# Optimization experiments

Hardware: AMD Instinct MI355X
Metric: run time of the kernel (lower is better)

## Reference

```python
import jax, jax.numpy as jnp
import numpy as np

N_EMBD = 1024
N_HEADS = 16
HEAD_DIM = N_EMBD // N_HEADS


def setup_inputs() -> dict:
    key = jax.random.key(0)
    ks = jax.random.split(key, 6)
    s = 1.0 / np.sqrt(N_EMBD)
    x = jax.random.normal(ks[0], (2, 2048, N_EMBD), dtype=jnp.float32)
    # torch Linear weights are [out, in]; y = x @ W.T
    Wk = jax.random.uniform(ks[1], (N_EMBD, N_EMBD), jnp.float32, -s, s)
    Wq = jax.random.uniform(ks[2], (N_EMBD, N_EMBD), jnp.float32, -s, s)
    Wv = jax.random.uniform(ks[3], (N_EMBD, N_EMBD), jnp.float32, -s, s)
    Wp = jax.random.uniform(ks[4], (N_EMBD, N_EMBD), jnp.float32, -s, s)
    bp = jax.random.uniform(ks[5], (N_EMBD,), jnp.float32, -s, s)
    return {"x": x, "Wq": Wq, "Wk": Wk, "Wv": Wv, "Wp": Wp, "bp": bp}


def reference(x, Wq, Wk, Wv, Wp, bp):
    B, T, C = x.shape
    H, D = N_HEADS, HEAD_DIM
    # projections (torch Linear: x @ W.T), reshape to [B, H, T, D]
    q = (x @ Wq.T).reshape(B, T, H, D).transpose(0, 2, 1, 3)
    k = (x @ Wk.T).reshape(B, T, H, D).transpose(0, 2, 1, 3)
    v = (x @ Wv.T).reshape(B, T, H, D).transpose(0, 2, 1, 3)
    # scaled causal attention, full [B,H,T,T] scores (faithful to original)
    att = jnp.einsum('bhqd,bhkd->bhqk', q, k) * (D ** -0.5)
    causal = jnp.tril(jnp.ones((T, T), dtype=bool))
    att = jnp.where(causal[None, None], att, -jnp.inf)
    att = jax.nn.softmax(att, axis=-1)
    out = jnp.einsum('bhqk,bhkd->bhqd', att, v)
    out = out.transpose(0, 2, 1, 3).reshape(B, T, C)
    return out @ Wp.T + bp
```

## Files before the change

kernel.cpp:

```cpp
#include <hip/hip_runtime.h>

typedef __bf16 bf16;
typedef __bf16 bf16x8 __attribute__((ext_vector_type(8)));
typedef float f32x4 __attribute__((ext_vector_type(4)));

typedef __attribute__((address_space(1))) const void as1_void;
typedef __attribute__((address_space(3))) void as3_void;

#define DEV __device__ __forceinline__
#define NEG_BIG (-1.0e30f)


DEV void async_load16(const void* g, void* l) {
  __builtin_amdgcn_global_load_lds((as1_void*)g, (as3_void*)l, 16, 0, 0);
}
DEV bf16x8 load8(const bf16* p) { bf16x8 v; __builtin_memcpy(&v, p, 16); return v; }
DEV void store8(bf16* p, bf16x8 v) { __builtin_memcpy(p, &v, 16); }
DEV float fexp2(float x) { float r; asm("v_exp_f32 %0, %1" : "=v"(r) : "v"(x)); return r; }

DEV int sniff_bf16(const unsigned short* __restrict__ xr) {
  const int lane = threadIdx.x & 63;
  const unsigned short w = xr[lane * 2];
  const int e = (w >> 7) & 0xFF;
  const bool sane = ((w & 0x7FFF) == 0) || (e >= 97 && e <= 157);
  return __popcll(__ballot(sane)) >= 48;
}

struct ConvArgs {
  const void* src[6];
  bf16* dst[6];
  int n[6];
};

__global__ __launch_bounds__(256) void convert_kernel(ConvArgs a) {
  const int isbf = sniff_bf16((const unsigned short*)a.src[0]);
  const int t = blockIdx.y;
  const int n = a.n[t];
  bf16* d = a.dst[t];
  const int stride = gridDim.x * 256 * 8;
  if (isbf) {
    const bf16* s = (const bf16*)a.src[t];
    for (int i = (blockIdx.x * 256 + threadIdx.x) * 8; i < n; i += stride)
      store8(d + i, load8(s + i));
  } else {
    const float* s = (const float*)a.src[t];
    for (int i = (blockIdx.x * 256 + threadIdx.x) * 8; i < n; i += stride) {
      float tmp[8];
      __builtin_memcpy(tmp, s + i, 32);
      bf16x8 v;
#pragma unroll
      for (int j = 0; j < 8; ++j) v[j] = (bf16)tmp[j];
      store8(d + i, v);
    }
  }
}

DEV void gemm_core_128_p(const bf16* A, const bf16* W, const int K, int m0, int n0,
                         f32x4 (&acc)[4][4]) {
  __shared__ alignas(16) bf16 As[3][128 * 32];
  __shared__ alignas(16) bf16 Bs[3][128 * 32];
  const int tid = threadIdx.x;
  const int lane = tid & 63;
  const int wid = tid >> 6;
  const int wm = (wid >> 1) << 6;
  const int wn = (wid & 1) << 6;
  const int lr = lane & 15;
  const int lg = lane >> 4;

  size_t srcA[2], srcB[2];
  int ldsoff[2];
#pragma unroll
  for (int it = 0; it < 2; ++it) {
    const int lin = it * 256 + tid;
    const int lr2 = lin >> 3, c = lin & 7;
    const int u = c ^ (lr2 & 7);
    const int r = lr2 * 2 + (u >> 2);
    const int g = u & 3;
    srcA[it] = (size_t)(m0 + r) * K + (size_t)(g * 8);
    srcB[it] = (size_t)(n0 + r) * K + (size_t)(g * 8);
    ldsoff[it] = lin * 8;
  }
  int offA[4], offB[4];
#pragma unroll
  for (int i = 0; i < 4; ++i) {
    const int r = wm + i * 16 + lr;
    const int cc = (lg | ((r & 1) << 2)) ^ ((r >> 1) & 7);
    offA[i] = (((r >> 1) << 3) | cc) * 8;
  }
#pragma unroll
  for (int j = 0; j < 4; ++j) {
    const int r = wn + j * 16 + lr;
    const int cc = (lg | ((r & 1) << 2)) ^ ((r >> 1) & 7);
    offB[j] = (((r >> 1) << 3) | cc) * 8;
  }

  const f32x4 zero = {0.f, 0.f, 0.f, 0.f};
#pragma unroll
  for (int i = 0; i < 4; ++i)
#pragma unroll
    for (int j = 0; j < 4; ++j) acc[i][j] = zero;

  const int nt = K >> 5;

  auto stage = [&](int buf, int t) {
    const size_t k0 = (size_t)(t << 5);
#pragma unroll
    for (int it = 0; it < 2; ++it) {
      async_load16(A + srcA[it] + k0, &As[buf][0] + ldsoff[it]);
      async_load16(W + srcB[it] + k0, &Bs[buf][0] + ldsoff[it]);
    }
  };

  auto compute = [&](int buf) {
    const bf16* as = &As[buf][0];
    const bf16* bs = &Bs[buf][0];
    bf16x8 af[4], bfr[4];
#pragma unroll
    for (int i = 0; i < 4; ++i) af[i] = load8(as + offA[i]);
#pragma unroll
    for (int j = 0; j < 4; ++j) bfr[j] = load8(bs + offB[j]);
    __builtin_amdgcn_s_setprio(1);
#pragma unroll
    for (int i = 0; i < 4; ++i)
#pragma unroll
      for (int j = 0; j < 4; ++j)
        acc[i][j] = __builtin_amdgcn_mfma_f32_16x16x32_bf16(af[i], bfr[j], acc[i][j], 0, 0, 0);
    __builtin_amdgcn_s_setprio(0);
  };

  stage(0, 0);
  stage(1, 1);
  int b0 = 0, b1 = 1, b2 = 2;
  for (int t = 0; t < nt; ++t) {
    if (t + 1 < nt) asm volatile("s_waitcnt vmcnt(4)" ::: "memory");
    else            asm volatile("s_waitcnt vmcnt(0)" ::: "memory");
    __builtin_amdgcn_s_barrier();
    if (t + 2 < nt) stage(b2, t + 2);
    compute(b0);
    const int tmp = b0; b0 = b1; b1 = b2; b2 = tmp;
  }
}

DEV void gemm_core_128x64_p(const bf16* A, const bf16* W, const int K, int m0, int n0,
                            f32x4 (&acc)[4][2]) {
  __shared__ alignas(16) bf16 As[3][128 * 32];
  __shared__ alignas(16) bf16 Bs[3][64 * 32];
  const int tid = threadIdx.x;
  const int lane = tid & 63;
  const int wid = tid >> 6;
  const int wm = (wid >> 1) << 6;
  const int wn = (wid & 1) << 5;
  const int lr = lane & 15;
  const int lg = lane >> 4;

  size_t srcA[2], srcB;
  int ldsoffA[2], ldsoffB;
#pragma unroll
  for (int it = 0; it < 2; ++it) {
    const int lin = it * 256 + tid;
    const int lr2 = lin >> 3, c = lin & 7;
    const int u = c ^ (lr2 & 7);
    srcA[it] = (size_t)(m0 + lr2 * 2 + (u >> 2)) * K + (size_t)((u & 3) * 8);
    ldsoffA[it] = lin * 8;
  }
  {
    const int lin = tid;
    const int lr2 = lin >> 3, c = lin & 7;
    const int u = c ^ (lr2 & 7);
    srcB = (size_t)(n0 + lr2 * 2 + (u >> 2)) * K + (size_t)((u & 3) * 8);
    ldsoffB = lin * 8;
  }
  int offA[4], offB[2];
#pragma unroll
  for (int i = 0; i < 4; ++i) {
    const int r = wm + i * 16 + lr;
    const int cc = (lg | ((r & 1) << 2)) ^ ((r >> 1) & 7);
    offA[i] = (((r >> 1) << 3) | cc) * 8;
  }
#pragma unroll
  for (int j = 0; j < 2; ++j) {
    const int r = wn + j * 16 + lr;
    const int cc = (lg | ((r & 1) << 2)) ^ ((r >> 1) & 7);
    offB[j] = (((r >> 1) << 3) | cc) * 8;
  }

  const f32x4 zero = {0.f, 0.f, 0.f, 0.f};
#pragma unroll
  for (int i = 0; i < 4; ++i)
#pragma unroll
    for (int j = 0; j < 2; ++j) acc[i][j] = zero;

  const int nt = K >> 5;

  auto stage = [&](int buf, int t) {
    const size_t k0 = (size_t)(t << 5);
#pragma unroll
    for (int it = 0; it < 2; ++it)
      async_load16(A + srcA[it] + k0, &As[buf][0] + ldsoffA[it]);
    async_load16(W + srcB + k0, &Bs[buf][0] + ldsoffB);
  };

  auto compute = [&](int buf) {
    const bf16* as = &As[buf][0];
    const bf16* bs = &Bs[buf][0];
    bf16x8 af[4], bfr[2];
#pragma unroll
    for (int i = 0; i < 4; ++i) af[i] = load8(as + offA[i]);
#pragma unroll
    for (int j = 0; j < 2; ++j) bfr[j] = load8(bs + offB[j]);
    __builtin_amdgcn_s_setprio(1);
#pragma unroll
    for (int i = 0; i < 4; ++i)
#pragma unroll
      for (int j = 0; j < 2; ++j)
        acc[i][j] = __builtin_amdgcn_mfma_f32_16x16x32_bf16(af[i], bfr[j], acc[i][j], 0, 0, 0);
    __builtin_amdgcn_s_setprio(0);
  };

  stage(0, 0);
  stage(1, 1);
  int b0 = 0, b1 = 1, b2 = 2;
  for (int t = 0; t < nt; ++t) {
    if (t + 1 < nt) asm volatile("s_waitcnt vmcnt(3)" ::: "memory");
    else            asm volatile("s_waitcnt vmcnt(0)" ::: "memory");
    __builtin_amdgcn_s_barrier();
    if (t + 2 < nt) stage(b2, t + 2);
    compute(b0);
    const int tmp = b0; b0 = b1; b1 = b2; b2 = tmp;
  }
}

DEV size_t frag_idx(int row, int col) {
  return ((size_t)(((col >> 5) * 4 + ((row >> 4) & 3)) * 64 + ((col >> 3) & 3) * 16 + (row & 15)) << 3)
         | (size_t)(col & 7);
}

__global__ __launch_bounds__(256) void qkv_proj_kernel(
    const bf16* __restrict__ x, const bf16* __restrict__ Wq,
    const bf16* __restrict__ Wk, const bf16* __restrict__ Wv,
    bf16* __restrict__ q_ws, bf16* __restrict__ k_ws, bf16* __restrict__ vt_ws) {
  const int L = blockIdx.x;
  const int xcd = L & 7;
  const int i2 = L >> 3;
  const int m0 = (xcd * 4 + (i2 & 3)) << 7;
  const int rest = i2 >> 2;
  const int n0 = (rest & 7) << 7;
  const int mode = rest >> 3;
  const bf16* W = (mode == 0) ? Wq : (mode == 1) ? Wk : Wv;
  f32x4 acc[4][4];
  gemm_core_128_p(x, W, 1024, m0, n0, acc);

  const int tid = threadIdx.x;
  const int lane = tid & 63, wid = tid >> 6;
  const int wm = (wid >> 1) << 6, wn = (wid & 1) << 6;
  const int lr = lane & 15, lg = lane >> 4;
  bf16* out = (mode == 0) ? q_ws : (mode == 1) ? k_ws : vt_ws;
  const float scale = (mode == 0) ? 0.18033688011112042f : 1.0f;
#pragma unroll
  for (int i = 0; i < 4; ++i) {
#pragma unroll
    for (int r = 0; r < 4; ++r) {
      const int m = m0 + wm + i * 16 + lg * 4 + r;
      const int b = m >> 11, t = m & 2047;
#pragma unroll
      for (int j = 0; j < 4; ++j) {
        const int n = n0 + wn + j * 16 + lr;
        const int h = n >> 6, d = n & 63;
        const float v = acc[i][j][r] * scale;
        const size_t base = ((size_t)(b * 16 + h) << 17) + ((size_t)(t >> 6) << 12);
        const size_t idx = base + ((mode < 2) ? frag_idx(t & 63, d) : frag_idx(d, t & 63));
        out[idx] = (bf16)v;
      }
    }
  }
}

__global__ __launch_bounds__(256, 4) void attn_kernel(
    const bf16* __restrict__ q_ws, const bf16* __restrict__ k_ws,
    const bf16* __restrict__ vt_ws, bf16* __restrict__ a_ws) {
  const int L = blockIdx.x;
  const int bh = (L & 7) * 4 + ((L >> 3) & 3);
  const int qt = 31 - (L >> 5);
  const int tid = threadIdx.x;
  const int lane = tid & 63, w = tid >> 6;
  const int lr = lane & 15, lg = lane >> 4;
  const int fo = lg * 16 + lr;

  __shared__ alignas(16) bf16 Ks[2][4096];
  __shared__ alignas(16) bf16 Ps[4][16 * 72];
  bf16* ps = &Ps[w][0];

  const size_t hb = (size_t)bh << 17;
  const int b = bh >> 4, h = bh & 15;
  const f32x4 zero = {0.f, 0.f, 0.f, 0.f};
  const bf16* kbase = k_ws + hb;
  const bf16* vbase = vt_ws + hb;
  const size_t qtb = hb + ((size_t)qt << 12);

  bf16x8 aq[2];
#pragma unroll
  for (int c2 = 0; c2 < 2; ++c2)
    aq[c2] = load8(q_ws + qtb + (size_t)(((c2 * 4 + w) * 64 + fo) << 3));

  f32x4 o_acc[4];
#pragma unroll
  for (int j = 0; j < 4; ++j) o_acc[j] = zero;
  float lsum[4] = {0.f, 0.f, 0.f, 0.f};

  const int nt = qt + 1;
  auto ktof = [&](int s) { return (s == 0) ? qt : (s - 1); };

  auto stage = [&](int buf, int s) {
    const int kt = ktof(s);
    const bf16* kg = kbase + ((size_t)kt << 12);
#pragma unroll
    for (int it = 0; it < 2; ++it) {
      const int lin = it * 256 + tid;
      async_load16(kg + lin * 8, &Ks[buf][0] + lin * 8);
    }
  };

  auto step = [&](int buf, int kt, bool diag) {
    const bf16* ks = &Ks[buf][0];
    const bf16* vg = vbase + ((size_t)kt << 12);
    bf16x8 bv[2][4];
#pragma unroll
    for (int c2 = 0; c2 < 2; ++c2)
#pragma unroll
      for (int j = 0; j < 4; ++j)
        bv[c2][j] = load8(vg + (size_t)(((c2 * 4 + j) * 64 + fo) << 3));

    f32x4 s[4];
    __builtin_amdgcn_s_setprio(1);
#pragma unroll
    for (int j = 0; j < 4; ++j) {
      s[j] = __builtin_amdgcn_mfma_f32_16x16x32_bf16(
          aq[0], load8(ks + (size_t)(((0 * 4 + j) * 64 + fo) << 3)), zero, 0, 0, 0);
      s[j] = __builtin_amdgcn_mfma_f32_16x16x32_bf16(
          aq[1], load8(ks + (size_t)(((1 * 4 + j) * 64 + fo) << 3)), s[j], 0, 0, 0);
    }
    __builtin_amdgcn_s_setprio(0);
    float p[4][4];
#pragma unroll
    for (int j = 0; j < 4; ++j) {
#pragma unroll
      for (int r = 0; r < 4; ++r) {
        float v = s[j][r];
        if (diag && (j * 16 + lr) > (w * 16 + lg * 4 + r)) v = NEG_BIG;
        p[j][r] = fexp2(v);
      }
    }
#pragma unroll
    for (int r = 0; r < 4; ++r)
      lsum[r] += (p[0][r] + p[1][r]) + (p[2][r] + p[3][r]);
#pragma unroll
    for (int j = 0; j < 4; ++j)
#pragma unroll
      for (int r = 0; r < 4; ++r)
        ps[(lg * 4 + r) * 72 + j * 16 + lr] = (bf16)p[j][r];
    __builtin_amdgcn_s_setprio(1);
#pragma unroll
    for (int c2 = 0; c2 < 2; ++c2) {
      const bf16x8 ap = load8(ps + lr * 72 + c2 * 32 + lg * 8);
#pragma unroll
      for (int j = 0; j < 4; ++j)
        o_acc[j] = __builtin_amdgcn_mfma_f32_16x16x32_bf16(ap, bv[c2][j], o_acc[j], 0, 0, 0);
    }
    __builtin_amdgcn_s_setprio(0);
  };

  stage(0, 0);
  int cur = 0;
  for (int t = 0; t < nt; ++t) {
    asm volatile("s_waitcnt vmcnt(0)" ::: "memory");
    __builtin_amdgcn_s_barrier();
    if (t + 1 < nt) stage(cur ^ 1, t + 1);
    step(cur, ktof(t), t == 0);
    cur ^= 1;
  }

#pragma unroll
  for (int r = 0; r < 4; ++r) {
    float v = lsum[r];
#pragma unroll
    for (int off = 1; off < 16; off <<= 1) v += __shfl_xor(v, off, 64);
    const float inv = 1.f / v;
    const int t = qt * 64 + w * 16 + lg * 4 + r;
#pragma unroll
    for (int j = 0; j < 4; ++j) {
      const size_t idx = (((size_t)(b * 2048 + t)) << 10) | (size_t)(h * 64 + j * 16 + lr);
      a_ws[idx] = (bf16)(o_acc[j][r] * inv);
    }
  }
}

__global__ __launch_bounds__(256) void out_proj_kernel(
    const bf16* __restrict__ A, const bf16* __restrict__ Wp,
    const bf16* __restrict__ bp, void* __restrict__ out,
    const unsigned short* __restrict__ xraw) {
  const int L = blockIdx.x;
  const int xcd = L & 7;
  const int i2 = L >> 3;
  const int m0 = (xcd * 4 + (i2 & 3)) << 7;
  const int n0 = (i2 >> 2) << 6;
  f32x4 acc[4][2];
  gemm_core_128x64_p(A, Wp, 1024, m0, n0, acc);

  const int tid = threadIdx.x;
  const int lane = tid & 63, wid = tid >> 6;
  const int wm = (wid >> 1) << 6, wn = (wid & 1) << 5;
  const int lr = lane & 15, lg = lane >> 4;
  const int isbf = sniff_bf16(xraw);
#pragma unroll
  for (int i = 0; i < 4; ++i) {
#pragma unroll
    for (int r = 0; r < 4; ++r) {
      const int m = m0 + wm + i * 16 + lg * 4 + r;
#pragma unroll
      for (int j = 0; j < 2; ++j) {
        const int n = n0 + wn + j * 16 + lr;
        const float v = acc[i][j][r] + (float)bp[n];
        const size_t idx = ((size_t)m << 10) | (size_t)n;
        if (isbf) ((bf16*)out)[idx] = (bf16)v;
        else      ((float*)out)[idx] = v;
      }
    }
  }
}

extern "C" void kernel_launch(void* const* d_in, const int* in_sizes, int n_in,
                              void* d_out, int out_size, void* d_ws, size_t ws_size,
                              hipStream_t stream) {
  (void)in_sizes; (void)n_in; (void)out_size;
  if (ws_size < (50u << 20)) return;

  char* ws = (char*)d_ws;
  bf16* q_ws  = (bf16*)(ws);
  bf16* k_ws  = (bf16*)(ws + (8u << 20));
  bf16* vt_ws = (bf16*)(ws + (16u << 20));
  bf16* a_ws  = (bf16*)(ws + (24u << 20));
  bf16* xc    = (bf16*)(ws + (32u << 20));
  bf16* Wqc   = (bf16*)(ws + (40u << 20));
  bf16* Wkc   = (bf16*)(ws + (42u << 20));
  bf16* Wvc   = (bf16*)(ws + (44u << 20));
  bf16* Wpc   = (bf16*)(ws + (46u << 20));
  bf16* bpc   = (bf16*)(ws + (48u << 20));

  ConvArgs ca;
  ca.src[0] = d_in[0]; ca.dst[0] = xc;  ca.n[0] = 4096 * 1024;
  ca.src[1] = d_in[1]; ca.dst[1] = Wqc; ca.n[1] = 1024 * 1024;
  ca.src[2] = d_in[2]; ca.dst[2] = Wkc; ca.n[2] = 1024 * 1024;
  ca.src[3] = d_in[3]; ca.dst[3] = Wvc; ca.n[3] = 1024 * 1024;
  ca.src[4] = d_in[4]; ca.dst[4] = Wpc; ca.n[4] = 1024 * 1024;
  ca.src[5] = d_in[5]; ca.dst[5] = bpc; ca.n[5] = 1024;
  convert_kernel<<<dim3(512, 6), 256, 0, stream>>>(ca);

  qkv_proj_kernel<<<768, 256, 0, stream>>>(xc, Wqc, Wkc, Wvc, q_ws, k_ws, vt_ws);
  attn_kernel<<<1024, 256, 0, stream>>>(q_ws, k_ws, vt_ws, a_ws);
  out_proj_kernel<<<512, 256, 0, stream>>>(a_ws, Wpc, bpc, d_out,
                                           (const unsigned short*)d_in[0]);
}
```

Baseline: 178.4 us.

## Fuse Q, K, V projections into one block sharing each x tile

```diff
diff --git a/kernel.cpp b/kernel.cpp
--- a/kernel.cpp
+++ b/kernel.cpp
@@ -55,92 +55,6 @@
   }
 }
 
-DEV void gemm_core_128_p(const bf16* A, const bf16* W, const int K, int m0, int n0,
-                         f32x4 (&acc)[4][4]) {
-  __shared__ alignas(16) bf16 As[3][128 * 32];
-  __shared__ alignas(16) bf16 Bs[3][128 * 32];
-  const int tid = threadIdx.x;
-  const int lane = tid & 63;
-  const int wid = tid >> 6;
-  const int wm = (wid >> 1) << 6;
-  const int wn = (wid & 1) << 6;
-  const int lr = lane & 15;
-  const int lg = lane >> 4;
-
-  size_t srcA[2], srcB[2];
-  int ldsoff[2];
-#pragma unroll
-  for (int it = 0; it < 2; ++it) {
-    const int lin = it * 256 + tid;
-    const int lr2 = lin >> 3, c = lin & 7;
-    const int u = c ^ (lr2 & 7);
-    const int r = lr2 * 2 + (u >> 2);
-    const int g = u & 3;
-    srcA[it] = (size_t)(m0 + r) * K + (size_t)(g * 8);
-    srcB[it] = (size_t)(n0 + r) * K + (size_t)(g * 8);
-    ldsoff[it] = lin * 8;
-  }
-  int offA[4], offB[4];
-#pragma unroll
-  for (int i = 0; i < 4; ++i) {
-    const int r = wm + i * 16 + lr;
-    const int cc = (lg | ((r & 1) << 2)) ^ ((r >> 1) & 7);
-    offA[i] = (((r >> 1) << 3) | cc) * 8;
-  }
-#pragma unroll
-  for (int j = 0; j < 4; ++j) {
-    const int r = wn + j * 16 + lr;
-    const int cc = (lg | ((r & 1) << 2)) ^ ((r >> 1) & 7);
-    offB[j] = (((r >> 1) << 3) | cc) * 8;
-  }
-
-  const f32x4 zero = {0.f, 0.f, 0.f, 0.f};
-#pragma unroll
-  for (int i = 0; i < 4; ++i)
-#pragma unroll
-    for (int j = 0; j < 4; ++j) acc[i][j] = zero;
-
-  const int nt = K >> 5;
-
-  auto stage = [&](int buf, int t) {
-    const size_t k0 = (size_t)(t << 5);
-#pragma unroll
-    for (int it = 0; it < 2; ++it) {
-      async_load16(A + srcA[it] + k0, &As[buf][0] + ldsoff[it]);
-      async_load16(W + srcB[it] + k0, &Bs[buf][0] + ldsoff[it]);
-    }
-  };
-
-  auto compute = [&](int buf) {
-    const bf16* as = &As[buf][0];
-    const bf16* bs = &Bs[buf][0];
-    bf16x8 af[4], bfr[4];
-#pragma unroll
-    for (int i = 0; i < 4; ++i) af[i] = load8(as + offA[i]);
-#pragma unroll
-    for (int j = 0; j < 4; ++j) bfr[j] = load8(bs + offB[j]);
-    __builtin_amdgcn_s_setprio(1);
-#pragma unroll
-    for (int i = 0; i < 4; ++i)
-#pragma unroll
-      for (int j = 0; j < 4; ++j)
-        acc[i][j] = __builtin_amdgcn_mfma_f32_16x16x32_bf16(af[i], bfr[j], acc[i][j], 0, 0, 0);
-    __builtin_amdgcn_s_setprio(0);
-  };
-
-  stage(0, 0);
-  stage(1, 1);
-  int b0 = 0, b1 = 1, b2 = 2;
-  for (int t = 0; t < nt; ++t) {
-    if (t + 1 < nt) asm volatile("s_waitcnt vmcnt(4)" ::: "memory");
-    else            asm volatile("s_waitcnt vmcnt(0)" ::: "memory");
-    __builtin_amdgcn_s_barrier();
-    if (t + 2 < nt) stage(b2, t + 2);
-    compute(b0);
-    const int tmp = b0; b0 = b1; b1 = b2; b2 = tmp;
-  }
-}
-
 DEV void gemm_core_128x64_p(const bf16* A, const bf16* W, const int K, int m0, int n0,
                             f32x4 (&acc)[4][2]) {
   __shared__ alignas(16) bf16 As[3][128 * 32];
@@ -235,7 +149,7 @@
          | (size_t)(col & 7);
 }
 
-__global__ __launch_bounds__(256) void qkv_proj_kernel(
+__global__ __launch_bounds__(256, 1) void qkv_proj_kernel(
     const bf16* __restrict__ x, const bf16* __restrict__ Wq,
     const bf16* __restrict__ Wk, const bf16* __restrict__ Wv,
     bf16* __restrict__ q_ws, bf16* __restrict__ k_ws, bf16* __restrict__ vt_ws) {
@@ -243,33 +157,117 @@
   const int xcd = L & 7;
   const int i2 = L >> 3;
   const int m0 = (xcd * 4 + (i2 & 3)) << 7;
-  const int rest = i2 >> 2;
-  const int n0 = (rest & 7) << 7;
-  const int mode = rest >> 3;
-  const bf16* W = (mode == 0) ? Wq : (mode == 1) ? Wk : Wv;
-  f32x4 acc[4][4];
-  gemm_core_128_p(x, W, 1024, m0, n0, acc);
+  const int n0 = (i2 >> 2) << 7;
+
+  __shared__ alignas(16) bf16 lds[2][4][128 * 32];
 
   const int tid = threadIdx.x;
-  const int lane = tid & 63, wid = tid >> 6;
-  const int wm = (wid >> 1) << 6, wn = (wid & 1) << 6;
-  const int lr = lane & 15, lg = lane >> 4;
-  bf16* out = (mode == 0) ? q_ws : (mode == 1) ? k_ws : vt_ws;
-  const float scale = (mode == 0) ? 0.18033688011112042f : 1.0f;
+  const int lane = tid & 63;
+  const int wid = tid >> 6;
+  const int wm = (wid >> 1) << 6;
+  const int wn = (wid & 1) << 6;
+  const int lr = lane & 15;
+  const int lg = lane >> 4;
+
+  const int K = 1024;
+  size_t srcA[2], srcB[2];
+  int ldsoff[2];
+#pragma unroll
+  for (int it = 0; it < 2; ++it) {
+    const int lin = it * 256 + tid;
+    const int lr2 = lin >> 3, c = lin & 7;
+    const int u = c ^ (lr2 & 7);
+    const int r = lr2 * 2 + (u >> 2);
+    const int g = u & 3;
+    srcA[it] = (size_t)(m0 + r) * K + (size_t)(g * 8);
+    srcB[it] = (size_t)(n0 + r) * K + (size_t)(g * 8);
+    ldsoff[it] = lin * 8;
+  }
+  int offA[4], offB[4];
 #pragma unroll
   for (int i = 0; i < 4; ++i) {
-#pragma unroll
-    for (int r = 0; r < 4; ++r) {
-      const int m = m0 + wm + i * 16 + lg * 4 + r;
-      const int b = m >> 11, t = m & 2047;
-#pragma unroll
-      for (int j = 0; j < 4; ++j) {
-        const int n = n0 + wn + j * 16 + lr;
-        const int h = n >> 6, d = n & 63;
-        const float v = acc[i][j][r] * scale;
-        const size_t base = ((size_t)(b * 16 + h) << 17) + ((size_t)(t >> 6) << 12);
-        const size_t idx = base + ((mode < 2) ? frag_idx(t & 63, d) : frag_idx(d, t & 63));
-        out[idx] = (bf16)v;
+    const int r = wm + i * 16 + lr;
+    const int cc = (lg | ((r & 1) << 2)) ^ ((r >> 1) & 7);
+    offA[i] = (((r >> 1) << 3) | cc) * 8;
+  }
+#pragma unroll
+  for (int j = 0; j < 4; ++j) {
+    const int r = wn + j * 16 + lr;
+    const int cc = (lg | ((r & 1) << 2)) ^ ((r >> 1) & 7);
+    offB[j] = (((r >> 1) << 3) | cc) * 8;
+  }
+
+  const bf16* Ws[3] = {Wq, Wk, Wv};
+  f32x4 acc[3][4][4];
+  const f32x4 zero = {0.f, 0.f, 0.f, 0.f};
+#pragma unroll
+  for (int mm = 0; mm < 3; ++mm)
+#pragma unroll
+    for (int i = 0; i < 4; ++i)
+#pragma unroll
+      for (int j = 0; j < 4; ++j) acc[mm][i][j] = zero;
+
+  const int nt = K >> 5;
+
+  auto stage = [&](int buf, int t) {
+    const size_t k0 = (size_t)(t << 5);
+#pragma unroll
+    for (int it = 0; it < 2; ++it) {
+      async_load16(x + srcA[it] + k0, &lds[buf][0][0] + ldsoff[it]);
+#pragma unroll
+      for (int mm = 0; mm < 3; ++mm)
+        async_load16(Ws[mm] + srcB[it] + k0, &lds[buf][1 + mm][0] + ldsoff[it]);
+    }
+  };
+
+  auto compute = [&](int buf) {
+    bf16x8 af[4];
+#pragma unroll
+    for (int i = 0; i < 4; ++i) af[i] = load8(&lds[buf][0][0] + offA[i]);
+#pragma unroll
+    for (int mm = 0; mm < 3; ++mm) {
+      bf16x8 bfr[4];
+#pragma unroll
+      for (int j = 0; j < 4; ++j) bfr[j] = load8(&lds[buf][1 + mm][0] + offB[j]);
+      __builtin_amdgcn_s_setprio(1);
+#pragma unroll
+      for (int i = 0; i < 4; ++i)
+#pragma unroll
+        for (int j = 0; j < 4; ++j)
+          acc[mm][i][j] = __builtin_amdgcn_mfma_f32_16x16x32_bf16(af[i], bfr[j], acc[mm][i][j], 0, 0, 0);
+      __builtin_amdgcn_s_setprio(0);
+    }
+  };
+
+  stage(0, 0);
+  int cur = 0;
+  for (int t = 0; t < nt; ++t) {
+    asm volatile("s_waitcnt vmcnt(0)" ::: "memory");
+    __builtin_amdgcn_s_barrier();
+    if (t + 1 < nt) stage(cur ^ 1, t + 1);
+    compute(cur);
+    cur ^= 1;
+  }
+
+#pragma unroll
+  for (int mm = 0; mm < 3; ++mm) {
+    bf16* out = (mm == 0) ? q_ws : (mm == 1) ? k_ws : vt_ws;
+    const float scale = (mm == 0) ? 0.18033688011112042f : 1.0f;
+#pragma unroll
+    for (int i = 0; i < 4; ++i) {
+#pragma unroll
+      for (int r = 0; r < 4; ++r) {
+        const int m = m0 + wm + i * 16 + lg * 4 + r;
+        const int b = m >> 11, t = m & 2047;
+#pragma unroll
+        for (int j = 0; j < 4; ++j) {
+          const int n = n0 + wn + j * 16 + lr;
+          const int h = n >> 6, d = n & 63;
+          const float v = acc[mm][i][j][r] * scale;
+          const size_t base = ((size_t)(b * 16 + h) << 17) + ((size_t)(t >> 6) << 12);
+          const size_t idx = base + ((mm < 2) ? frag_idx(t & 63, d) : frag_idx(d, t & 63));
+          out[idx] = (bf16)v;
+        }
       }
     }
   }
@@ -455,7 +453,7 @@
   ca.src[5] = d_in[5]; ca.dst[5] = bpc; ca.n[5] = 1024;
   convert_kernel<<<dim3(512, 6), 256, 0, stream>>>(ca);
 
-  qkv_proj_kernel<<<768, 256, 0, stream>>>(xc, Wqc, Wkc, Wvc, q_ws, k_ws, vt_ws);
+  qkv_proj_kernel<<<256, 256, 0, stream>>>(xc, Wqc, Wkc, Wvc, q_ws, k_ws, vt_ws);
   attn_kernel<<<1024, 256, 0, stream>>>(q_ws, k_ws, vt_ws, a_ws);
   out_proj_kernel<<<512, 256, 0, stream>>>(a_ws, Wpc, bpc, d_out,
                                            (const unsigned short*)d_in[0]);
```

Measured after the change: 197.1 us. 10.5% more time.
